# Performance work log

Hardware: AMD Instinct MI355X
Metric: run time of the kernel (lower is better)

Reference implementation:

```python
import jax, jax.numpy as jnp
import numpy as np

EPS = 1e-08


def setup_inputs() -> dict:
    key = jax.random.key(0)
    k1, k2 = jax.random.split(key)
    x = jax.random.normal(k1, (8192, 4096), dtype=jnp.float32)
    # xavier-uniform-ish init for weight (faithful scale; exact init irrelevant to math)
    limit = float(np.sqrt(6.0 / (4096 + 4096)))
    weight = jax.random.uniform(k2, (4096, 4096), dtype=jnp.float32, minval=-limit, maxval=limit)
    mask = jnp.ones((4096, 4096), dtype=jnp.float32)
    bias = jnp.zeros((4096,), dtype=jnp.float32)
    return {"x": x, "weight": weight, "mask": mask, "bias": bias}


def reference(x, weight, mask, bias):
    # masked weights
    mw = weight * mask  # [out, in]
    aw = jnp.abs(mw)
    # per-call global stats (training mode, adaptive threshold)
    scale = aw.mean() + EPS
    threshold = jnp.std(aw, ddof=1) * 0.5  # torch .std() is unbiased
    # ternary {-1, 0, +1} then rescale
    tern = jnp.where(mw > threshold, 1.0, 0.0) + jnp.where(mw < -threshold, -1.0, 0.0)
    tw = tern * scale
    # F.linear: x @ W^T + b
    return jnp.einsum("bi,oi->bo", x, tw) + bias
```

## Files before the change

### kernel.cpp

```cpp
#include <hip/hip_runtime.h>
#include <stdint.h>

#define M_DIM 8192
#define N_DIM 4096
#define K_DIM 4096
#define NW (N_DIM * K_DIM)
#define RM_BLOCKS 2048

typedef __bf16 bf16x8 __attribute__((ext_vector_type(8)));
typedef float  floatx4 __attribute__((ext_vector_type(4)));
typedef unsigned short u16;
typedef unsigned int   u32;

__global__ void reduce_moments(const float* __restrict__ w,
                               const float* __restrict__ msk,
                               double* __restrict__ part) {
    const int nv = NW / 4;
    const int stride = gridDim.x * blockDim.x;
    int idx = blockIdx.x * blockDim.x + threadIdx.x;
    float s1 = 0.f, s2 = 0.f;
    const float4* w4 = (const float4*)w;
    const float4* m4 = (const float4*)msk;
    for (int i = idx; i < nv; i += stride) {
        float4 a = w4[i];
        float4 b = m4[i];
        float p0 = fabsf(a.x * b.x), p1 = fabsf(a.y * b.y);
        float p2 = fabsf(a.z * b.z), p3 = fabsf(a.w * b.w);
        s1 += p0 + p1 + p2 + p3;
        s2 += p0 * p0 + p1 * p1 + p2 * p2 + p3 * p3;
    }
    double d1 = (double)s1, d2 = (double)s2;
    #pragma unroll
    for (int off = 32; off > 0; off >>= 1) {
        d1 += __shfl_down(d1, off);
        d2 += __shfl_down(d2, off);
    }
    __shared__ double sh[8];
    int lane = threadIdx.x & 63;
    int wv = threadIdx.x >> 6;
    if (lane == 0) { sh[wv] = d1; sh[wv + 4] = d2; }
    __syncthreads();
    if (threadIdx.x == 0) {
        part[blockIdx.x]             = sh[0] + sh[1] + sh[2] + sh[3];
        part[RM_BLOCKS + blockIdx.x] = sh[4] + sh[5] + sh[6] + sh[7];
    }
}

__global__ void finalize_stats(const double* __restrict__ part, float* __restrict__ st) {
    double s1 = 0.0, s2 = 0.0;
    for (int i = threadIdx.x; i < RM_BLOCKS; i += 256) {
        s1 += part[i];
        s2 += part[RM_BLOCKS + i];
    }
    #pragma unroll
    for (int off = 32; off > 0; off >>= 1) {
        s1 += __shfl_down(s1, off);
        s2 += __shfl_down(s2, off);
    }
    __shared__ double sh[8];
    int lane = threadIdx.x & 63;
    int wv = threadIdx.x >> 6;
    if (lane == 0) { sh[wv] = s1; sh[wv + 4] = s2; }
    __syncthreads();
    if (threadIdx.x == 0) {
        double S1 = sh[0] + sh[1] + sh[2] + sh[3];
        double S2 = sh[4] + sh[5] + sh[6] + sh[7];
        const double n = (double)NW;
        double mean = S1 / n;
        double var = (S2 - S1 * S1 / n) / (n - 1.0);
        st[0] = (float)(mean + 1e-8);
        st[1] = (float)(0.5 * sqrt(var));
    }
}

__device__ __forceinline__ u16 f2bf(float f) {
    u32 u = __float_as_uint(f);
    u += 0x7FFFu + ((u >> 16) & 1u);
    return (u16)(u >> 16);
}

__global__ void tern_cvt(const float* __restrict__ w, const float* __restrict__ msk,
                         const float* __restrict__ st, u16* __restrict__ tw,
                         const float* __restrict__ x, u16* __restrict__ xbf) {
    const int b = blockIdx.x;
    if (b < NW / 2048) {
        const float thr = st[1];
        const int i = (b * 256 + threadIdx.x) * 8;
        float4 a0 = *(const float4*)(w + i);
        float4 a1 = *(const float4*)(w + i + 4);
        float4 b0 = *(const float4*)(msk + i);
        float4 b1 = *(const float4*)(msk + i + 4);
        float p[8] = {a0.x * b0.x, a0.y * b0.y, a0.z * b0.z, a0.w * b0.w,
                      a1.x * b1.x, a1.y * b1.y, a1.z * b1.z, a1.w * b1.w};
        union { u16 u[8]; uint4 v; } r;
        #pragma unroll
        for (int j = 0; j < 8; ++j)
            r.u[j] = p[j] > thr ? (u16)0x3F80 : (p[j] < -thr ? (u16)0xBF80 : (u16)0);
        *(uint4*)(tw + i) = r.v;
    } else {
        const int i = ((b - NW / 2048) * 256 + threadIdx.x) * 8;
        float4 a0 = *(const float4*)(x + i);
        float4 a1 = *(const float4*)(x + i + 4);
        union { u16 u[8]; uint4 v; } r;
        r.u[0] = f2bf(a0.x); r.u[1] = f2bf(a0.y); r.u[2] = f2bf(a0.z); r.u[3] = f2bf(a0.w);
        r.u[4] = f2bf(a1.x); r.u[5] = f2bf(a1.y); r.u[6] = f2bf(a1.z); r.u[7] = f2bf(a1.w);
        *(uint4*)(xbf + i) = r.v;
    }
}

__device__ __forceinline__ void gld16(const __bf16* g, __bf16* l) {
    __builtin_amdgcn_global_load_lds(
        (__attribute__((address_space(1))) void*)g,
        (__attribute__((address_space(3))) void*)l, 16, 0, 0);
}


#define BARRIER __builtin_amdgcn_s_barrier()
#define LGK0    asm volatile("s_waitcnt lgkmcnt(0)" ::: "memory")
#define VMC4    asm volatile("s_waitcnt vmcnt(4)" ::: "memory")

#define STAGE_A(ktn, dst)                                           \
    gld16(gA[0] + (ktn) * 64, sh + (dst) + (0 * 8 + wv) * 512);     \
    gld16(gA[1] + (ktn) * 64, sh + (dst) + (1 * 8 + wv) * 512);     \
    gld16(gA[2] + (ktn) * 64, sh + (dst) + (2 * 8 + wv) * 512);     \
    gld16(gA[3] + (ktn) * 64, sh + (dst) + (3 * 8 + wv) * 512);

#define STAGE_BH(ktn, dst, h)                                                   \
    gld16(gB[(h) * 2 + 0] + (ktn) * 64, sh + (dst) + ((h) * 16 + wv * 2 + 0) * 512); \
    gld16(gB[(h) * 2 + 1] + (ktn) * 64, sh + (dst) + ((h) * 16 + wv * 2 + 1) * 512);

#define PHASE(pidx, aCur, STAGE_CODE)                                           \
    {                                                                           \
        bf16x8 af[2][2];                                                        \
        _Pragma("unroll")                                                       \
        for (int mi = 0; mi < 2; ++mi)                                          \
            _Pragma("unroll")                                                   \
            for (int ks = 0; ks < 2; ++ks)                                      \
                af[mi][ks] = *(const bf16x8*)(sh + (aCur) +                     \
                    ((rsA + (pidx) * 2 + mi) * 2 + ks) * 512 + laneElem);       \
        STAGE_CODE                                                              \
        BARRIER;                                                                \
        LGK0;                                                                   \
        __builtin_amdgcn_s_setprio(1);                                          \
        _Pragma("unroll")                                                       \
        for (int mi = 0; mi < 2; ++mi)                                          \
            _Pragma("unroll")                                                   \
            for (int ni = 0; ni < 4; ++ni)                                      \
                _Pragma("unroll")                                               \
                for (int ks = 0; ks < 2; ++ks)                                  \
                    acc[(pidx) * 2 + mi][ni] =                                  \
                        __builtin_amdgcn_mfma_f32_16x16x32_bf16(                \
                            af[mi][ks], bfr[ni][ks], acc[(pidx) * 2 + mi][ni],  \
                            0, 0, 0);                                           \
        __builtin_amdgcn_s_setprio(0);                                          \
    }

#define TILE(P, kt)                                                             \
    {                                                                           \
        const int aCur = (P) * 16384;                                           \
        const int aNxt = ((P) ^ 1) * 16384;                                     \
        const int bCur = 32768 + (P) * 16384;                                   \
        const int kt1 = ((kt) + 1) & 63;                                        \
        const int kt2 = ((kt) + 2) & 63;                                        \
        _Pragma("unroll")                                                       \
        for (int ni = 0; ni < 4; ++ni)                                          \
            _Pragma("unroll")                                                   \
            for (int ks = 0; ks < 2; ++ks)                                      \
                bfr[ni][ks] = *(const bf16x8*)(sh + bCur +                      \
                    ((rsB + ni) * 2 + ks) * 512 + laneElem);                    \
        PHASE(0, aCur, STAGE_A(kt1, aNxt))                                      \
        BARRIER;                                                                \
        PHASE(1, aCur, STAGE_BH(kt2, bCur, 0))                                  \
        BARRIER;                                                                \
        PHASE(2, aCur, STAGE_BH(kt2, bCur, 1))                                  \
        BARRIER;                                                                \
        PHASE(3, aCur, ;)                                                       \
        VMC4;                                                                   \
        BARRIER;                                                                \
    }

__global__ __launch_bounds__(512, 2) void gemm_tern(
        const __bf16* __restrict__ A, const __bf16* __restrict__ B,
        const float* __restrict__ bias, const float* __restrict__ st,
        float* __restrict__ C) {
    __shared__ __bf16 sh[65536];

    const int t = threadIdx.x;
    const int lane = t & 63;
    const int wv = t >> 6;
    const int wm = (wv >> 2) * 128;
    const int wn = (wv & 3) * 64;
    const int bm = blockIdx.y * 256;
    const int bn = blockIdx.x * 256;

    const int laneElem = ((lane & 15) << 5) +
                         (((lane >> 4) << 3) ^ ((lane & 8) << 1));
    const int rsA = wm >> 4;
    const int rsB = wn >> 4;

    const int lp = lane ^ ((lane & 32) >> 4);
    const int srow = lp >> 2;
    const int scol = (lp & 3) * 8;

    const __bf16* gA[4];
    #pragma unroll
    for (int i = 0; i < 4; ++i) {
        int stA = i * 8 + wv;
        gA[i] = A + (size_t)(bm + (stA >> 1) * 16 + srow) * K_DIM +
                (stA & 1) * 32 + scol;
    }
    const __bf16* gB[4];
    #pragma unroll
    for (int j = 0; j < 2; ++j) {
        int st0 = wv * 2 + j;
        gB[j] = B + (size_t)(bn + (st0 >> 1) * 16 + srow) * K_DIM +
                (st0 & 1) * 32 + scol;
        int st1 = 16 + wv * 2 + j;
        gB[2 + j] = B + (size_t)(bn + (st1 >> 1) * 16 + srow) * K_DIM +
                    (st1 & 1) * 32 + scol;
    }

    floatx4 acc[8][4] = {};
    bf16x8 bfr[4][2];

    STAGE_A(0, 0)
    STAGE_BH(0, 32768, 0)
    STAGE_BH(0, 32768, 1)
    STAGE_BH(1, 32768 + 16384, 0)
    STAGE_BH(1, 32768 + 16384, 1)
    VMC4;
    BARRIER;

    #pragma unroll 1
    for (int t2 = 0; t2 < 64; t2 += 2) {
        TILE(0, t2)
        TILE(1, t2 + 1)
    }

    const float scale = st[0];
    const int rbase = bm + wm + ((lane >> 4) << 2);
    const int cbase = bn + wn + (lane & 15);
    #pragma unroll
    for (int ni = 0; ni < 4; ++ni) {
        const int col = cbase + ni * 16;
        const float bv = bias[col];
        #pragma unroll
        for (int mi = 0; mi < 8; ++mi) {
            const int row = rbase + mi * 16;
            #pragma unroll
            for (int rg = 0; rg < 4; ++rg)
                C[(size_t)(row + rg) * N_DIM + col] = acc[mi][ni][rg] * scale + bv;
        }
    }
}

extern "C" void kernel_launch(void* const* d_in, const int* in_sizes, int n_in,
                              void* d_out, int out_size, void* d_ws, size_t ws_size,
                              hipStream_t stream) {
    const float* x    = (const float*)d_in[0];
    const float* w    = (const float*)d_in[1];
    const float* msk  = (const float*)d_in[2];
    const float* bias = (const float*)d_in[3];
    float* out = (float*)d_out;

    char* ws = (char*)d_ws;
    float*  st   = (float*)(ws + 64);
    double* part = (double*)(ws + 256);
    u16*    tern = (u16*)(ws + 256);
    u16*    xbf  = (u16*)(ws + 256 + (size_t)NW * 2);

    reduce_moments<<<RM_BLOCKS, 256, 0, stream>>>(w, msk, part);
    finalize_stats<<<1, 256, 0, stream>>>(part, st);
    tern_cvt<<<NW / 2048 + (M_DIM * K_DIM) / 2048, 256, 0, stream>>>(
        w, msk, st, tern, x, xbf);

    dim3 grid(N_DIM / 256, M_DIM / 256);
    gemm_tern<<<grid, 512, 0, stream>>>((const __bf16*)xbf, (const __bf16*)tern,
                                        bias, st, out);
}
```

Before: 537.6 us.

## Fuse weight-moment reduction with x conversion and swizzle GEMM tiles per XCD

Adds a prep kernel that converts x to bf16 and computes the masked-weight moments in the same grid-stride pass. It also stores the masked product w*mask to a workspace buffer, so the ternarize pass reads one array instead of two. The GEMM block index is remapped so consecutive blocks going to the same XCD cover contiguous tile rows, which aims for better L2 reuse of A and B tiles. The new path needs extra workspace and falls back to the old kernels when the workspace is too small; total bytes moved in preprocessing stay roughly the same.

After: 558.8 us. 4.0% more time.

```diff
diff --git a/kernel.cpp b/kernel.cpp
--- a/kernel.cpp
+++ b/kernel.cpp
@@ -11,6 +11,79 @@
 typedef float  floatx4 __attribute__((ext_vector_type(4)));
 typedef unsigned short u16;
 typedef unsigned int   u32;
+
+__device__ __forceinline__ u16 f2bf(float f) {
+    u32 u = __float_as_uint(f);
+    u += 0x7FFFu + ((u >> 16) & 1u);
+    return (u16)(u >> 16);
+}
+
+__device__ __forceinline__ void block_reduce2(double d1, double d2,
+                                              double* out1, double* out2) {
+    #pragma unroll
+    for (int off = 32; off > 0; off >>= 1) {
+        d1 += __shfl_down(d1, off);
+        d2 += __shfl_down(d2, off);
+    }
+    __shared__ double sh[8];
+    int lane = threadIdx.x & 63;
+    int wv = threadIdx.x >> 6;
+    if (lane == 0) { sh[wv] = d1; sh[wv + 4] = d2; }
+    __syncthreads();
+    if (threadIdx.x == 0) {
+        *out1 = sh[0] + sh[1] + sh[2] + sh[3];
+        *out2 = sh[4] + sh[5] + sh[6] + sh[7];
+    }
+}
+
+__global__ void prep(const float* __restrict__ w, const float* __restrict__ msk,
+                     const float* __restrict__ x, float* __restrict__ p,
+                     u16* __restrict__ xbf, double* __restrict__ part) {
+    const int stride = gridDim.x * blockDim.x;
+    const int idx = blockIdx.x * blockDim.x + threadIdx.x;
+
+    const int nx = (M_DIM * K_DIM) / 8;
+    for (int i = idx; i < nx; i += stride) {
+        float4 a0 = *(const float4*)(x + i * 8);
+        float4 a1 = *(const float4*)(x + i * 8 + 4);
+        union { u16 u[8]; uint4 v; } r;
+        r.u[0] = f2bf(a0.x); r.u[1] = f2bf(a0.y); r.u[2] = f2bf(a0.z); r.u[3] = f2bf(a0.w);
+        r.u[4] = f2bf(a1.x); r.u[5] = f2bf(a1.y); r.u[6] = f2bf(a1.z); r.u[7] = f2bf(a1.w);
+        *(uint4*)(xbf + i * 8) = r.v;
+    }
+
+    const int nv = NW / 4;
+    float s1 = 0.f, s2 = 0.f;
+    const float4* w4 = (const float4*)w;
+    const float4* m4 = (const float4*)msk;
+    float4* p4 = (float4*)p;
+    for (int i = idx; i < nv; i += stride) {
+        float4 a = w4[i];
+        float4 b = m4[i];
+        float4 pr;
+        pr.x = a.x * b.x; pr.y = a.y * b.y; pr.z = a.z * b.z; pr.w = a.w * b.w;
+        p4[i] = pr;
+        float q0 = fabsf(pr.x), q1 = fabsf(pr.y), q2 = fabsf(pr.z), q3 = fabsf(pr.w);
+        s1 += q0 + q1 + q2 + q3;
+        s2 += q0 * q0 + q1 * q1 + q2 * q2 + q3 * q3;
+    }
+    block_reduce2((double)s1, (double)s2,
+                  &part[blockIdx.x], &part[RM_BLOCKS + blockIdx.x]);
+}
+
+__global__ void ternarize_p(const float* __restrict__ p, const float* __restrict__ st,
+                            u16* __restrict__ tw) {
+    const float thr = st[1];
+    const int i = (blockIdx.x * blockDim.x + threadIdx.x) * 8;
+    float4 a0 = *(const float4*)(p + i);
+    float4 a1 = *(const float4*)(p + i + 4);
+    float pv[8] = {a0.x, a0.y, a0.z, a0.w, a1.x, a1.y, a1.z, a1.w};
+    union { u16 u[8]; uint4 v; } r;
+    #pragma unroll
+    for (int j = 0; j < 8; ++j)
+        r.u[j] = pv[j] > thr ? (u16)0x3F80 : (pv[j] < -thr ? (u16)0xBF80 : (u16)0);
+    *(uint4*)(tw + i) = r.v;
+}
 
 __global__ void reduce_moments(const float* __restrict__ w,
                                const float* __restrict__ msk,
@@ -29,54 +102,8 @@
         s1 += p0 + p1 + p2 + p3;
         s2 += p0 * p0 + p1 * p1 + p2 * p2 + p3 * p3;
     }
-    double d1 = (double)s1, d2 = (double)s2;
-    #pragma unroll
-    for (int off = 32; off > 0; off >>= 1) {
-        d1 += __shfl_down(d1, off);
-        d2 += __shfl_down(d2, off);
-    }
-    __shared__ double sh[8];
-    int lane = threadIdx.x & 63;
-    int wv = threadIdx.x >> 6;
-    if (lane == 0) { sh[wv] = d1; sh[wv + 4] = d2; }
-    __syncthreads();
-    if (threadIdx.x == 0) {
-        part[blockIdx.x]             = sh[0] + sh[1] + sh[2] + sh[3];
-        part[RM_BLOCKS + blockIdx.x] = sh[4] + sh[5] + sh[6] + sh[7];
-    }
-}
-
-__global__ void finalize_stats(const double* __restrict__ part, float* __restrict__ st) {
-    double s1 = 0.0, s2 = 0.0;
-    for (int i = threadIdx.x; i < RM_BLOCKS; i += 256) {
-        s1 += part[i];
-        s2 += part[RM_BLOCKS + i];
-    }
-    #pragma unroll
-    for (int off = 32; off > 0; off >>= 1) {
-        s1 += __shfl_down(s1, off);
-        s2 += __shfl_down(s2, off);
-    }
-    __shared__ double sh[8];
-    int lane = threadIdx.x & 63;
-    int wv = threadIdx.x >> 6;
-    if (lane == 0) { sh[wv] = s1; sh[wv + 4] = s2; }
-    __syncthreads();
-    if (threadIdx.x == 0) {
-        double S1 = sh[0] + sh[1] + sh[2] + sh[3];
-        double S2 = sh[4] + sh[5] + sh[6] + sh[7];
-        const double n = (double)NW;
-        double mean = S1 / n;
-        double var = (S2 - S1 * S1 / n) / (n - 1.0);
-        st[0] = (float)(mean + 1e-8);
-        st[1] = (float)(0.5 * sqrt(var));
-    }
-}
-
-__device__ __forceinline__ u16 f2bf(float f) {
-    u32 u = __float_as_uint(f);
-    u += 0x7FFFu + ((u >> 16) & 1u);
-    return (u16)(u >> 16);
+    block_reduce2((double)s1, (double)s2,
+                  &part[blockIdx.x], &part[RM_BLOCKS + blockIdx.x]);
 }
 
 __global__ void tern_cvt(const float* __restrict__ w, const float* __restrict__ msk,
@@ -108,6 +135,33 @@
     }
 }
 
+__global__ void finalize_stats(const double* __restrict__ part, float* __restrict__ st) {
+    double s1 = 0.0, s2 = 0.0;
+    for (int i = threadIdx.x; i < RM_BLOCKS; i += 256) {
+        s1 += part[i];
+        s2 += part[RM_BLOCKS + i];
+    }
+    #pragma unroll
+    for (int off = 32; off > 0; off >>= 1) {
+        s1 += __shfl_down(s1, off);
+        s2 += __shfl_down(s2, off);
+    }
+    __shared__ double sh[8];
+    int lane = threadIdx.x & 63;
+    int wv = threadIdx.x >> 6;
+    if (lane == 0) { sh[wv] = s1; sh[wv + 4] = s2; }
+    __syncthreads();
+    if (threadIdx.x == 0) {
+        double S1 = sh[0] + sh[1] + sh[2] + sh[3];
+        double S2 = sh[4] + sh[5] + sh[6] + sh[7];
+        const double n = (double)NW;
+        double mean = S1 / n;
+        double var = (S2 - S1 * S1 / n) / (n - 1.0);
+        st[0] = (float)(mean + 1e-8);
+        st[1] = (float)(0.5 * sqrt(var));
+    }
+}
+
 __device__ __forceinline__ void gld16(const __bf16* g, __bf16* l) {
     __builtin_amdgcn_global_load_lds(
         (__attribute__((address_space(1))) void*)g,
@@ -190,8 +244,11 @@
     const int wv = t >> 6;
     const int wm = (wv >> 2) * 128;
     const int wn = (wv & 3) * 64;
-    const int bm = blockIdx.y * 256;
-    const int bn = blockIdx.x * 256;
+
+    const int flat = blockIdx.y * gridDim.x + blockIdx.x;
+    const int nf = (flat & 7) * 64 + (flat >> 3);
+    const int bm = (nf >> 4) * 256;
+    const int bn = (nf & 15) * 256;
 
     const int laneElem = ((lane & 15) << 5) +
                          (((lane >> 4) << 3) ^ ((lane & 8) << 1));
@@ -268,11 +325,21 @@
     double* part = (double*)(ws + 256);
     u16*    tern = (u16*)(ws + 256);
     u16*    xbf  = (u16*)(ws + 256 + (size_t)NW * 2);
-
-    reduce_moments<<<RM_BLOCKS, 256, 0, stream>>>(w, msk, part);
-    finalize_stats<<<1, 256, 0, stream>>>(part, st);
-    tern_cvt<<<NW / 2048 + (M_DIM * K_DIM) / 2048, 256, 0, stream>>>(
-        w, msk, st, tern, x, xbf);
+    float*  p    = (float*)(ws + 256 + (size_t)NW * 2 + (size_t)M_DIM * K_DIM * 2);
+
+    const size_t need_p = 256 + (size_t)NW * 2 + (size_t)M_DIM * K_DIM * 2
+                          + (size_t)NW * 4;
+
+    if (ws_size >= need_p) {
+        prep<<<RM_BLOCKS, 256, 0, stream>>>(w, msk, x, p, xbf, part);
+        finalize_stats<<<1, 256, 0, stream>>>(part, st);
+        ternarize_p<<<NW / 2048, 256, 0, stream>>>(p, st, tern);
+    } else {
+        reduce_moments<<<RM_BLOCKS, 256, 0, stream>>>(w, msk, part);
+        finalize_stats<<<1, 256, 0, stream>>>(part, st);
+        tern_cvt<<<NW / 2048 + (M_DIM * K_DIM) / 2048, 256, 0, stream>>>(
+            w, msk, st, tern, x, xbf);
+    }
 
     dim3 grid(N_DIM / 256, M_DIM / 256);
     gemm_tern<<<grid, 512, 0, stream>>>((const __bf16*)xbf, (const __bf16*)tern,
```
